# Optimization experiments

Measured on AMD Instinct MI355X. Metric: run time of the kernel, lower is better.

The kernel has to match this reference:

```python
import jax, jax.numpy as jnp
import numpy as np

E = 64        # num_local_experts
N = 32768     # total permuted tokens
H = 1024      # hidden_dim
F = 1024      # intermediate_dim
C = N // E    # per-expert capacity (setup uses equal token counts)


def setup_inputs() -> dict:
    key = jax.random.key(0)
    k1, k2, k3, k4 = jax.random.split(key, 4)
    s = 0.02  # init scale
    return {
        "permuted_local_hidden_states": jax.random.normal(k1, (N, H), jnp.float32),
        "tokens_per_expert": jnp.full((E,), C, dtype=jnp.int32),
        "w_gate": jax.random.normal(k2, (E, H, F), jnp.float32) * s,
        "w_up": jax.random.normal(k3, (E, H, F), jnp.float32) * s,
        "w_down": jax.random.normal(k4, (E, F, H), jnp.float32) * s,
    }


def reference(permuted_local_hidden_states, tokens_per_expert, w_gate, w_up, w_down):
    x = permuted_local_hidden_states  # [N, H], sorted by expert
    counts = tokens_per_expert.astype(jnp.int32)  # [E]
    # start offset of each expert's contiguous token range (torch cumsum + cat([0]))
    starts = jnp.concatenate([jnp.zeros((1,), jnp.int32), jnp.cumsum(counts)])[:-1]
    # expert id and within-expert position for every token (jit-friendly dispatch)
    eid = jnp.repeat(jnp.arange(E, dtype=jnp.int32), counts, total_repeat_length=N)
    pos = jnp.arange(N, dtype=jnp.int32) - starts[eid]
    # gather tokens into fixed-capacity per-expert buffer [E, C, H]; unused slots stay 0
    buf = jnp.zeros((E, C, H), x.dtype).at[eid, pos].set(x)
    # grouped LLaMA MLP: down( silu(gate(x)) * up(x) ), one GEMM triple per expert, batched
    gate = jnp.einsum('ech,ehf->ecf', buf, w_gate)
    up = jnp.einsum('ech,ehf->ecf', buf, w_up)
    h = jax.nn.silu(gate) * up                      # [E, C, F]
    out_buf = jnp.einsum('ecf,efh->ech', h, w_down)  # [E, C, H]
    # scatter back to flat token order (output_local[start:end] = output)
    output_local = out_buf[eid, pos]  # [N, H]
    return output_local
```

## Files before the change

### kernel.cpp

```cpp
#include <hip/hip_runtime.h>
#include <stdint.h>


#define NUM_E 64
#define DIM_H 1024
#define DIM_F 1024
#define CAP   512
#define NTOK  32768

typedef short short8 __attribute__((ext_vector_type(8)));
typedef float f32x4 __attribute__((ext_vector_type(4)));

#define VMCNT(n)  asm volatile("s_waitcnt vmcnt(" #n ")" ::: "memory")
#define LGKMCNT0  asm volatile("s_waitcnt lgkmcnt(0)" ::: "memory")
#define SBAR      __builtin_amdgcn_s_barrier()
#define SCHED0    __builtin_amdgcn_sched_barrier(0)

__device__ __forceinline__ uint32_t cvtpk(float lo, float hi) {
  uint32_t r;
  asm("v_cvt_pk_bf16_f32 %0, %1, %2" : "=v"(r) : "v"(lo), "v"(hi));
  return r;
}
__device__ __forceinline__ unsigned short f2bf(float a) {
  uint32_t ua = __builtin_bit_cast(uint32_t, a);
  ua += 0x7FFFu + ((ua >> 16) & 1u);
  return (unsigned short)(ua >> 16);
}
__device__ __forceinline__ void gload_lds16(const void* g, void* l) {
  __builtin_amdgcn_global_load_lds((const __attribute__((address_space(1))) uint32_t*)g,
                                   (__attribute__((address_space(3))) uint32_t*)l, 16, 0, 0);
}

__global__ __launch_bounds__(256) void cvt_kernel(const float* __restrict__ x,
                                                  unsigned short* __restrict__ xbf) {
  size_t i = ((size_t)blockIdx.x * 256 + threadIdx.x) * 8;
  f32x4 a = *reinterpret_cast<const f32x4*>(x + i);
  f32x4 b = *reinterpret_cast<const f32x4*>(x + i + 4);
  int4 o = make_int4((int)cvtpk(a[0], a[1]), (int)cvtpk(a[2], a[3]),
                     (int)cvtpk(b[0], b[1]), (int)cvtpk(b[2], b[3]));
  *reinterpret_cast<int4*>(xbf + i) = o;
}

__global__ __launch_bounds__(512, 2) void gateup_kernel_v3(
    const unsigned short* __restrict__ xbf, const float* __restrict__ wg,
    const float* __restrict__ wu, unsigned short* __restrict__ hout)
{
  __shared__ unsigned char smem[131072];
  const int t = threadIdx.x;
  int bid = blockIdx.x;
  bid = (bid & 7) * 128 + (bid >> 3);
  const int e = bid >> 4, rr = bid & 15, mb = rr >> 3, nb = rr & 7;
  const int row0 = e * CAP + mb * 256;
  const int col0 = nb * 128;
  const unsigned short* Ag = xbf + (size_t)row0 * DIM_H;
  const float* Bgg = wg + (size_t)e * (DIM_H * DIM_F) + col0;
  const float* Bug = wu + (size_t)e * (DIM_H * DIM_F) + col0;

  const int lane = t & 63, wid = t >> 6;
  const int wm = wid >> 1, wn = wid & 1;

  f32x4 accg[4][4], accu[4][4];
  #pragma unroll
  for (int i = 0; i < 4; i++)
    #pragma unroll
    for (int j = 0; j < 4; j++) {
      accg[i][j] = f32x4{0.f, 0.f, 0.f, 0.f};
      accu[i][j] = f32x4{0.f, 0.f, 0.f, 0.f};
    }

  const int bn = t & 127, bkb = (t >> 7) * 16;
  float bg[16], bu[16];

  auto loadB = [&](int k0) {
    #pragma unroll
    for (int i = 0; i < 16; i++) {
      bg[i] = Bgg[(size_t)(k0 + bkb + i) * DIM_F + bn];
      bu[i] = Bug[(size_t)(k0 + bkb + i) * DIM_F + bn];
    }
  };
  auto writeB = [&](int b) {
    const int Bb = 65536 + b * 32768;
    #pragma unroll
    for (int j = 0; j < 4; j++) {
      int off = Bb + bn * 128 + (((bkb + j * 4) * 2) ^ ((bn & 7) << 4));
      *reinterpret_cast<uint2*>(&smem[off]) =
          make_uint2(cvtpk(bg[j*4+0], bg[j*4+1]), cvtpk(bg[j*4+2], bg[j*4+3]));
      *reinterpret_cast<uint2*>(&smem[off + 16384]) =
          make_uint2(cvtpk(bu[j*4+0], bu[j*4+1]), cvtpk(bu[j*4+2], bu[j*4+3]));
    }
  };
  auto loadA = [&](int k0, int buf) {
    #pragma unroll
    for (int j = 0; j < 4; j++) {
      int lin = (j * 512 + t) * 16;
      int r = lin >> 7;
      int q = (lin >> 4) & 7;
      const void* src = (const unsigned char*)Ag + (size_t)r * 2048 + k0 * 2 + ((q ^ (r & 7)) * 16);
      gload_lds16(src, &smem[buf * 32768 + lin]);
    }
  };
  auto compute = [&](int kt) {
    const int Ab = (kt & 1) * 32768;
    const int Bb = 65536 + (kt & 1) * 32768;
    __builtin_amdgcn_s_setprio(1);
    #pragma unroll
    for (int kk = 0; kk < 2; kk++) {
      short8 a[4], bgf[4], buf_[4];
      #pragma unroll
      for (int mi = 0; mi < 4; mi++) {
        int r = wm * 64 + mi * 16 + (lane & 15);
        a[mi] = *reinterpret_cast<const short8*>(
            &smem[Ab + r * 128 + ((kk * 64 + (lane >> 4) * 16) ^ ((r & 7) << 4))]);
      }
      #pragma unroll
      for (int ni = 0; ni < 4; ni++) {
        int n = wn * 64 + ni * 16 + (lane & 15);
        int off = Bb + n * 128 + ((kk * 64 + (lane >> 4) * 16) ^ ((n & 7) << 4));
        bgf[ni]  = *reinterpret_cast<const short8*>(&smem[off]);
        buf_[ni] = *reinterpret_cast<const short8*>(&smem[off + 16384]);
      }
      #pragma unroll
      for (int mi = 0; mi < 4; mi++)
        #pragma unroll
        for (int ni = 0; ni < 4; ni++) {
          accg[mi][ni] = __builtin_amdgcn_mfma_f32_16x16x32_bf16(a[mi], bgf[ni],  accg[mi][ni], 0, 0, 0);
          accu[mi][ni] = __builtin_amdgcn_mfma_f32_16x16x32_bf16(a[mi], buf_[ni], accu[mi][ni], 0, 0, 0);
        }
    }
    __builtin_amdgcn_s_setprio(0);
  };

  const int NT = DIM_H / 64;
  loadB(0);
  loadA(0, 0);
  VMCNT(4); SCHED0;
  writeB(0);
  LGKMCNT0; VMCNT(0); SCHED0;
  SBAR;
  for (int kt = 0; kt < NT; kt++) {
    if (kt + 1 < NT) {
      loadB((kt + 1) * 64);
      loadA((kt + 1) * 64, (kt + 1) & 1);
      SCHED0;
    }
    compute(kt);
    if (kt + 1 < NT) {
      VMCNT(4); SCHED0;
      writeB((kt + 1) & 1);
      LGKMCNT0; VMCNT(0); SCHED0;
      SBAR;
    }
  }

  #pragma unroll
  for (int mi = 0; mi < 4; mi++)
    #pragma unroll
    for (int ni = 0; ni < 4; ni++) {
      int col = col0 + wn * 64 + ni * 16 + (lane & 15);
      int rbase = row0 + wm * 64 + mi * 16 + (lane >> 4) * 4;
      #pragma unroll
      for (int j = 0; j < 4; j++) {
        float g = accg[mi][ni][j], u = accu[mi][ni][j];
        float hv = (g / (1.f + __expf(-g))) * u;
        hout[(size_t)(rbase + j) * DIM_F + col] = f2bf(hv);
      }
    }
}

__global__ __launch_bounds__(512, 2) void down_kernel_v3(
    const unsigned short* __restrict__ hin, const float* __restrict__ wd,
    float* __restrict__ out)
{
  __shared__ unsigned char smem[98304];
  const int t = threadIdx.x;
  int bid = blockIdx.x;
  bid = (bid & 7) * 128 + (bid >> 3);
  const int e = bid >> 4, rr = bid & 15, mb = rr >> 3, nb = rr & 7;
  const int row0 = e * CAP + mb * 256;
  const int col0 = nb * 128;
  const unsigned short* Ag = hin + (size_t)row0 * DIM_F;
  const float* Bdg = wd + (size_t)e * (DIM_F * DIM_H) + col0;

  const int lane = t & 63, wid = t >> 6;
  const int wm = wid >> 1, wn = wid & 1;

  f32x4 acc[4][4];
  #pragma unroll
  for (int i = 0; i < 4; i++)
    #pragma unroll
    for (int j = 0; j < 4; j++) acc[i][j] = f32x4{0.f, 0.f, 0.f, 0.f};

  const int bn = t & 127, bkb = (t >> 7) * 16;
  float bs[16];

  auto loadB = [&](int k0) {
    #pragma unroll
    for (int i = 0; i < 16; i++)
      bs[i] = Bdg[(size_t)(k0 + bkb + i) * DIM_H + bn];
  };
  auto writeB = [&](int b) {
    const int Bb = 65536 + b * 16384;
    #pragma unroll
    for (int j = 0; j < 4; j++) {
      int off = Bb + bn * 128 + (((bkb + j * 4) * 2) ^ ((bn & 7) << 4));
      *reinterpret_cast<uint2*>(&smem[off]) =
          make_uint2(cvtpk(bs[j*4+0], bs[j*4+1]), cvtpk(bs[j*4+2], bs[j*4+3]));
    }
  };
  auto loadA = [&](int k0, int buf) {
    #pragma unroll
    for (int j = 0; j < 4; j++) {
      int lin = (j * 512 + t) * 16;
      int r = lin >> 7;
      int q = (lin >> 4) & 7;
      const void* src = (const unsigned char*)Ag + (size_t)r * 2048 + k0 * 2 + ((q ^ (r & 7)) * 16);
      gload_lds16(src, &smem[buf * 32768 + lin]);
    }
  };
  auto compute = [&](int kt) {
    const int Ab = (kt & 1) * 32768;
    const int Bb = 65536 + (kt & 1) * 16384;
    __builtin_amdgcn_s_setprio(1);
    #pragma unroll
    for (int kk = 0; kk < 2; kk++) {
      short8 a[4], b[4];
      #pragma unroll
      for (int mi = 0; mi < 4; mi++) {
        int r = wm * 64 + mi * 16 + (lane & 15);
        a[mi] = *reinterpret_cast<const short8*>(
            &smem[Ab + r * 128 + ((kk * 64 + (lane >> 4) * 16) ^ ((r & 7) << 4))]);
      }
      #pragma unroll
      for (int ni = 0; ni < 4; ni++) {
        int n = wn * 64 + ni * 16 + (lane & 15);
        b[ni] = *reinterpret_cast<const short8*>(
            &smem[Bb + n * 128 + ((kk * 64 + (lane >> 4) * 16) ^ ((n & 7) << 4))]);
      }
      #pragma unroll
      for (int mi = 0; mi < 4; mi++)
        #pragma unroll
        for (int ni = 0; ni < 4; ni++)
          acc[mi][ni] = __builtin_amdgcn_mfma_f32_16x16x32_bf16(a[mi], b[ni], acc[mi][ni], 0, 0, 0);
    }
    __builtin_amdgcn_s_setprio(0);
  };

  const int NT = DIM_F / 64;
  loadB(0);
  loadA(0, 0);
  VMCNT(4); SCHED0;
  writeB(0);
  LGKMCNT0; VMCNT(0); SCHED0;
  SBAR;
  for (int kt = 0; kt < NT; kt++) {
    if (kt + 1 < NT) {
      loadB((kt + 1) * 64);
      loadA((kt + 1) * 64, (kt + 1) & 1);
      SCHED0;
    }
    compute(kt);
    if (kt + 1 < NT) {
      VMCNT(4); SCHED0;
      writeB((kt + 1) & 1);
      LGKMCNT0; VMCNT(0); SCHED0;
      SBAR;
    }
  }

  #pragma unroll
  for (int mi = 0; mi < 4; mi++)
    #pragma unroll
    for (int ni = 0; ni < 4; ni++) {
      int col = col0 + wn * 64 + ni * 16 + (lane & 15);
      int rbase = row0 + wm * 64 + mi * 16 + (lane >> 4) * 4;
      #pragma unroll
      for (int j = 0; j < 4; j++)
        out[(size_t)(rbase + j) * DIM_H + col] = acc[mi][ni][j];
    }
}

extern "C" void kernel_launch(void* const* d_in, const int* in_sizes, int n_in,
                              void* d_out, int out_size, void* d_ws, size_t ws_size,
                              hipStream_t stream) {
  (void)in_sizes; (void)n_in; (void)out_size; (void)ws_size;
  const float* x  = (const float*)d_in[0];
  const float* wg = (const float*)d_in[2];
  const float* wu = (const float*)d_in[3];
  const float* wd = (const float*)d_in[4];
  unsigned short* h   = (unsigned short*)d_ws;
  unsigned short* xbf = (unsigned short*)((char*)d_ws + (size_t)NTOK * DIM_F * 2);
  float* out = (float*)d_out;

  cvt_kernel<<<dim3((NTOK * DIM_H) / (256 * 8)), dim3(256), 0, stream>>>(x, xbf);
  gateup_kernel_v3<<<dim3(1024), dim3(512), 0, stream>>>(xbf, wg, wu, h);
  down_kernel_v3<<<dim3(1024), dim3(512), 0, stream>>>(h, wd, out);
}
```

Measured before the change: 365.2 us.

## Switch GEMMs to 32x32x16 MFMA and vectorize fp32 weight loads

Both GEMM kernels replace the 16x16x32 bf16 MFMA tiles with 32x32x16 tiles. Each wave now holds 2x2 accumulators of 16 floats, which cuts the number of LDS fragment reads per MFMA FLOP and raises MFMA efficiency. The fp32 weight loads change from scalar per-column loads to float4 vector loads over a 4x4 k-by-n patch, with a transposed write into LDS. The epilogue row and column mapping is rewritten to match the 32x32 output layout, so any mapping mistake would make the output wrong.

New measurement: 405.9 us. 1.11x slower.

```diff
diff --git a/kernel.cpp b/kernel.cpp
--- a/kernel.cpp
+++ b/kernel.cpp
@@ -10,6 +10,7 @@
 
 typedef short short8 __attribute__((ext_vector_type(8)));
 typedef float f32x4 __attribute__((ext_vector_type(4)));
+typedef float f32x16 __attribute__((ext_vector_type(16)));
 
 #define VMCNT(n)  asm volatile("s_waitcnt vmcnt(" #n ")" ::: "memory")
 #define LGKMCNT0  asm volatile("s_waitcnt lgkmcnt(0)" ::: "memory")
@@ -41,7 +42,7 @@
   *reinterpret_cast<int4*>(xbf + i) = o;
 }
 
-__global__ __launch_bounds__(512, 2) void gateup_kernel_v3(
+__global__ __launch_bounds__(512, 2) void gateup_kernel_v4(
     const unsigned short* __restrict__ xbf, const float* __restrict__ wg,
     const float* __restrict__ wu, unsigned short* __restrict__ hout)
 {
@@ -59,34 +60,36 @@
   const int lane = t & 63, wid = t >> 6;
   const int wm = wid >> 1, wn = wid & 1;
 
-  f32x4 accg[4][4], accu[4][4];
+  f32x16 accg[2][2], accu[2][2];
   #pragma unroll
-  for (int i = 0; i < 4; i++)
-    #pragma unroll
-    for (int j = 0; j < 4; j++) {
-      accg[i][j] = f32x4{0.f, 0.f, 0.f, 0.f};
-      accu[i][j] = f32x4{0.f, 0.f, 0.f, 0.f};
-    }
-
-  const int bn = t & 127, bkb = (t >> 7) * 16;
-  float bg[16], bu[16];
+  for (int i = 0; i < 2; i++)
+    #pragma unroll
+    for (int j = 0; j < 2; j++) {
+      accg[i][j] = (f32x16)(0.f);
+      accu[i][j] = (f32x16)(0.f);
+    }
+
+  const int kg = t & 15, ng = t >> 4;
+  f32x4 vg[4], vu[4];
 
   auto loadB = [&](int k0) {
     #pragma unroll
-    for (int i = 0; i < 16; i++) {
-      bg[i] = Bgg[(size_t)(k0 + bkb + i) * DIM_F + bn];
-      bu[i] = Bug[(size_t)(k0 + bkb + i) * DIM_F + bn];
+    for (int i = 0; i < 4; i++) {
+      size_t off = (size_t)(k0 + kg * 4 + i) * DIM_F + ng * 4;
+      vg[i] = *reinterpret_cast<const f32x4*>(Bgg + off);
+      vu[i] = *reinterpret_cast<const f32x4*>(Bug + off);
     }
   };
   auto writeB = [&](int b) {
     const int Bb = 65536 + b * 32768;
     #pragma unroll
     for (int j = 0; j < 4; j++) {
-      int off = Bb + bn * 128 + (((bkb + j * 4) * 2) ^ ((bn & 7) << 4));
+      int n = ng * 4 + j;
+      int off = Bb + n * 128 + ((kg * 8) ^ ((n & 7) << 4));
       *reinterpret_cast<uint2*>(&smem[off]) =
-          make_uint2(cvtpk(bg[j*4+0], bg[j*4+1]), cvtpk(bg[j*4+2], bg[j*4+3]));
+          make_uint2(cvtpk(vg[0][j], vg[1][j]), cvtpk(vg[2][j], vg[3][j]));
       *reinterpret_cast<uint2*>(&smem[off + 16384]) =
-          make_uint2(cvtpk(bu[j*4+0], bu[j*4+1]), cvtpk(bu[j*4+2], bu[j*4+3]));
+          make_uint2(cvtpk(vu[0][j], vu[1][j]), cvtpk(vu[2][j], vu[3][j]));
     }
   };
   auto loadA = [&](int k0, int buf) {
@@ -104,27 +107,28 @@
     const int Bb = 65536 + (kt & 1) * 32768;
     __builtin_amdgcn_s_setprio(1);
     #pragma unroll
-    for (int kk = 0; kk < 2; kk++) {
-      short8 a[4], bgf[4], buf_[4];
-      #pragma unroll
-      for (int mi = 0; mi < 4; mi++) {
-        int r = wm * 64 + mi * 16 + (lane & 15);
+    for (int kk = 0; kk < 4; kk++) {
+      const int kbyte = kk * 32 + (lane >> 5) * 16;
+      short8 a[2], bgf[2], buf_[2];
+      #pragma unroll
+      for (int mi = 0; mi < 2; mi++) {
+        int r = wm * 64 + mi * 32 + (lane & 31);
         a[mi] = *reinterpret_cast<const short8*>(
-            &smem[Ab + r * 128 + ((kk * 64 + (lane >> 4) * 16) ^ ((r & 7) << 4))]);
-      }
-      #pragma unroll
-      for (int ni = 0; ni < 4; ni++) {
-        int n = wn * 64 + ni * 16 + (lane & 15);
-        int off = Bb + n * 128 + ((kk * 64 + (lane >> 4) * 16) ^ ((n & 7) << 4));
-        bgf[ni]  = *reinterpret_cast<const short8*>(&smem[off]);
-        buf_[ni] = *reinterpret_cast<const short8*>(&smem[off + 16384]);
-      }
-      #pragma unroll
-      for (int mi = 0; mi < 4; mi++)
+            &smem[Ab + r * 128 + (kbyte ^ ((r & 7) << 4))]);
+      }
+      #pragma unroll
+      for (int nj = 0; nj < 2; nj++) {
+        int n = wn * 64 + nj * 32 + (lane & 31);
+        int off = Bb + n * 128 + (kbyte ^ ((n & 7) << 4));
+        bgf[nj]  = *reinterpret_cast<const short8*>(&smem[off]);
+        buf_[nj] = *reinterpret_cast<const short8*>(&smem[off + 16384]);
+      }
+      #pragma unroll
+      for (int mi = 0; mi < 2; mi++)
         #pragma unroll
-        for (int ni = 0; ni < 4; ni++) {
-          accg[mi][ni] = __builtin_amdgcn_mfma_f32_16x16x32_bf16(a[mi], bgf[ni],  accg[mi][ni], 0, 0, 0);
-          accu[mi][ni] = __builtin_amdgcn_mfma_f32_16x16x32_bf16(a[mi], buf_[ni], accu[mi][ni], 0, 0, 0);
+        for (int nj = 0; nj < 2; nj++) {
+          accg[mi][nj] = __builtin_amdgcn_mfma_f32_32x32x16_bf16(a[mi], bgf[nj],  accg[mi][nj], 0, 0, 0);
+          accu[mi][nj] = __builtin_amdgcn_mfma_f32_32x32x16_bf16(a[mi], buf_[nj], accu[mi][nj], 0, 0, 0);
         }
     }
     __builtin_amdgcn_s_setprio(0);
@@ -153,21 +157,22 @@
   }
 
   #pragma unroll
-  for (int mi = 0; mi < 4; mi++)
-    #pragma unroll
-    for (int ni = 0; ni < 4; ni++) {
-      int col = col0 + wn * 64 + ni * 16 + (lane & 15);
-      int rbase = row0 + wm * 64 + mi * 16 + (lane >> 4) * 4;
-      #pragma unroll
-      for (int j = 0; j < 4; j++) {
-        float g = accg[mi][ni][j], u = accu[mi][ni][j];
+  for (int mi = 0; mi < 2; mi++)
+    #pragma unroll
+    for (int nj = 0; nj < 2; nj++) {
+      int col = col0 + wn * 64 + nj * 32 + (lane & 31);
+      int rbase = row0 + wm * 64 + mi * 32 + 4 * (lane >> 5);
+      #pragma unroll
+      for (int reg = 0; reg < 16; reg++) {
+        int row = rbase + (reg & 3) + 8 * (reg >> 2);
+        float g = accg[mi][nj][reg], u = accu[mi][nj][reg];
         float hv = (g / (1.f + __expf(-g))) * u;
-        hout[(size_t)(rbase + j) * DIM_F + col] = f2bf(hv);
-      }
-    }
-}
-
-__global__ __launch_bounds__(512, 2) void down_kernel_v3(
+        hout[(size_t)row * DIM_F + col] = f2bf(hv);
+      }
+    }
+}
+
+__global__ __launch_bounds__(512, 2) void down_kernel_v4(
     const unsigned short* __restrict__ hin, const float* __restrict__ wd,
     float* __restrict__ out)
 {
@@ -184,27 +189,28 @@
   const int lane = t & 63, wid = t >> 6;
   const int wm = wid >> 1, wn = wid & 1;
 
-  f32x4 acc[4][4];
+  f32x16 acc[2][2];
   #pragma unroll
-  for (int i = 0; i < 4; i++)
-    #pragma unroll
-    for (int j = 0; j < 4; j++) acc[i][j] = f32x4{0.f, 0.f, 0.f, 0.f};
-
-  const int bn = t & 127, bkb = (t >> 7) * 16;
-  float bs[16];
+  for (int i = 0; i < 2; i++)
+    #pragma unroll
+    for (int j = 0; j < 2; j++) acc[i][j] = (f32x16)(0.f);
+
+  const int kg = t & 15, ng = t >> 4;
+  f32x4 vb[4];
 
   auto loadB = [&](int k0) {
     #pragma unroll
-    for (int i = 0; i < 16; i++)
-      bs[i] = Bdg[(size_t)(k0 + bkb + i) * DIM_H + bn];
+    for (int i = 0; i < 4; i++)
+      vb[i] = *reinterpret_cast<const f32x4*>(Bdg + (size_t)(k0 + kg * 4 + i) * DIM_H + ng * 4);
   };
   auto writeB = [&](int b) {
     const int Bb = 65536 + b * 16384;
     #pragma unroll
     for (int j = 0; j < 4; j++) {
-      int off = Bb + bn * 128 + (((bkb + j * 4) * 2) ^ ((bn & 7) << 4));
+      int n = ng * 4 + j;
+      int off = Bb + n * 128 + ((kg * 8) ^ ((n & 7) << 4));
       *reinterpret_cast<uint2*>(&smem[off]) =
-          make_uint2(cvtpk(bs[j*4+0], bs[j*4+1]), cvtpk(bs[j*4+2], bs[j*4+3]));
+          make_uint2(cvtpk(vb[0][j], vb[1][j]), cvtpk(vb[2][j], vb[3][j]));
     }
   };
   auto loadA = [&](int k0, int buf) {
@@ -222,25 +228,26 @@
     const int Bb = 65536 + (kt & 1) * 16384;
     __builtin_amdgcn_s_setprio(1);
     #pragma unroll
-    for (int kk = 0; kk < 2; kk++) {
-      short8 a[4], b[4];
-      #pragma unroll
-      for (int mi = 0; mi < 4; mi++) {
-        int r = wm * 64 + mi * 16 + (lane & 15);
+    for (int kk = 0; kk < 4; kk++) {
+      const int kbyte = kk * 32 + (lane >> 5) * 16;
+      short8 a[2], b[2];
+      #pragma unroll
+      for (int mi = 0; mi < 2; mi++) {
+        int r = wm * 64 + mi * 32 + (lane & 31);
         a[mi] = *reinterpret_cast<const short8*>(
-            &smem[Ab + r * 128 + ((kk * 64 + (lane >> 4) * 16) ^ ((r & 7) << 4))]);
-      }
-      #pragma unroll
-      for (int ni = 0; ni < 4; ni++) {
-        int n = wn * 64 + ni * 16 + (lane & 15);
-        b[ni] = *reinterpret_cast<const short8*>(
-            &smem[Bb + n * 128 + ((kk * 64 + (lane >> 4) * 16) ^ ((n & 7) << 4))]);
-      }
-      #pragma unroll
-      for (int mi = 0; mi < 4; mi++)
+            &smem[Ab + r * 128 + (kbyte ^ ((r & 7) << 4))]);
+      }
+      #pragma unroll
+      for (int nj = 0; nj < 2; nj++) {
+        int n = wn * 64 + nj * 32 + (lane & 31);
+        b[nj] = *reinterpret_cast<const short8*>(
+            &smem[Bb + n * 128 + (kbyte ^ ((n & 7) << 4))]);
+      }
+      #pragma unroll
+      for (int mi = 0; mi < 2; mi++)
         #pragma unroll
-        for (int ni = 0; ni < 4; ni++)
-          acc[mi][ni] = __builtin_amdgcn_mfma_f32_16x16x32_bf16(a[mi], b[ni], acc[mi][ni], 0, 0, 0);
+        for (int nj = 0; nj < 2; nj++)
+          acc[mi][nj] = __builtin_amdgcn_mfma_f32_32x32x16_bf16(a[mi], b[nj], acc[mi][nj], 0, 0, 0);
     }
     __builtin_amdgcn_s_setprio(0);
   };
@@ -268,14 +275,16 @@
   }
 
   #pragma unroll
-  for (int mi = 0; mi < 4; mi++)
-    #pragma unroll
-    for (int ni = 0; ni < 4; ni++) {
-      int col = col0 + wn * 64 + ni * 16 + (lane & 15);
-      int rbase = row0 + wm * 64 + mi * 16 + (lane >> 4) * 4;
-      #pragma unroll
-      for (int j = 0; j < 4; j++)
-        out[(size_t)(rbase + j) * DIM_H + col] = acc[mi][ni][j];
+  for (int mi = 0; mi < 2; mi++)
+    #pragma unroll
+    for (int nj = 0; nj < 2; nj++) {
+      int col = col0 + wn * 64 + nj * 32 + (lane & 31);
+      int rbase = row0 + wm * 64 + mi * 32 + 4 * (lane >> 5);
+      #pragma unroll
+      for (int reg = 0; reg < 16; reg++) {
+        int row = rbase + (reg & 3) + 8 * (reg >> 2);
+        out[(size_t)row * DIM_H + col] = acc[mi][nj][reg];
+      }
     }
 }
 
@@ -292,6 +301,6 @@
   float* out = (float*)d_out;
 
   cvt_kernel<<<dim3((NTOK * DIM_H) / (256 * 8)), dim3(256), 0, stream>>>(x, xbf);
-  gateup_kernel_v3<<<dim3(1024), dim3(512), 0, stream>>>(xbf, wg, wu, h);
-  down_kernel_v3<<<dim3(1024), dim3(512), 0, stream>>>(h, wd, out);
-}
+  gateup_kernel_v4<<<dim3(1024), dim3(512), 0, stream>>>(xbf, wg, wu, h);
+  down_kernel_v4<<<dim3(1024), dim3(512), 0, stream>>>(h, wd, out);
+}
```

## Load A fragments directly to registers and vectorize fp32 weight loads

Applied to the files above, without the earlier changes.

Both GEMM kernels stop staging the activation tile in LDS via global_load_lds and instead load A fragments straight from global memory into registers, double-buffered across two k-steps. The weight loads switch from scalar per-column loads to float4 loads along N, with a k-group by n-group thread mapping and a matching swizzled LDS write. This cuts the LDS footprint and LDS traffic and should make weight fetches more coalesced. In exchange it drops the explicit vmcnt/sched_barrier pipelining in favor of compiler scheduling and __syncthreads, raises register pressure, and A reads are no longer shared between warps in LDS, so the duplicated A traffic goes through the caches.

After: 1.251 ms. +242.5%, slower.

```diff
diff --git a/kernel.cpp b/kernel.cpp
--- a/kernel.cpp
+++ b/kernel.cpp
@@ -11,11 +11,6 @@
 typedef short short8 __attribute__((ext_vector_type(8)));
 typedef float f32x4 __attribute__((ext_vector_type(4)));
 
-#define VMCNT(n)  asm volatile("s_waitcnt vmcnt(" #n ")" ::: "memory")
-#define LGKMCNT0  asm volatile("s_waitcnt lgkmcnt(0)" ::: "memory")
-#define SBAR      __builtin_amdgcn_s_barrier()
-#define SCHED0    __builtin_amdgcn_sched_barrier(0)
-
 __device__ __forceinline__ uint32_t cvtpk(float lo, float hi) {
   uint32_t r;
   asm("v_cvt_pk_bf16_f32 %0, %1, %2" : "=v"(r) : "v"(lo), "v"(hi));
@@ -25,10 +20,6 @@
   uint32_t ua = __builtin_bit_cast(uint32_t, a);
   ua += 0x7FFFu + ((ua >> 16) & 1u);
   return (unsigned short)(ua >> 16);
-}
-__device__ __forceinline__ void gload_lds16(const void* g, void* l) {
-  __builtin_amdgcn_global_load_lds((const __attribute__((address_space(1))) uint32_t*)g,
-                                   (__attribute__((address_space(3))) uint32_t*)l, 16, 0, 0);
 }
 
 __global__ __launch_bounds__(256) void cvt_kernel(const float* __restrict__ x,
@@ -41,11 +32,11 @@
   *reinterpret_cast<int4*>(xbf + i) = o;
 }
 
-__global__ __launch_bounds__(512, 2) void gateup_kernel_v3(
+__global__ __launch_bounds__(512, 2) void gateup_kernel_v5(
     const unsigned short* __restrict__ xbf, const float* __restrict__ wg,
     const float* __restrict__ wu, unsigned short* __restrict__ hout)
 {
-  __shared__ unsigned char smem[131072];
+  __shared__ unsigned char smem[65536];
   const int t = threadIdx.x;
   int bid = blockIdx.x;
   bid = (bid & 7) * 128 + (bid >> 3);
@@ -68,50 +59,45 @@
       accu[i][j] = f32x4{0.f, 0.f, 0.f, 0.f};
     }
 
-  const int bn = t & 127, bkb = (t >> 7) * 16;
-  float bg[16], bu[16];
+  const int kg = t & 15, ng = t >> 4;
+  f32x4 vg[4], vu[4];
 
   auto loadB = [&](int k0) {
     #pragma unroll
-    for (int i = 0; i < 16; i++) {
-      bg[i] = Bgg[(size_t)(k0 + bkb + i) * DIM_F + bn];
-      bu[i] = Bug[(size_t)(k0 + bkb + i) * DIM_F + bn];
+    for (int i = 0; i < 4; i++) {
+      size_t off = (size_t)(k0 + kg * 4 + i) * DIM_F + ng * 4;
+      vg[i] = *reinterpret_cast<const f32x4*>(Bgg + off);
+      vu[i] = *reinterpret_cast<const f32x4*>(Bug + off);
     }
   };
   auto writeB = [&](int b) {
-    const int Bb = 65536 + b * 32768;
+    const int Bb = b * 32768;
     #pragma unroll
     for (int j = 0; j < 4; j++) {
-      int off = Bb + bn * 128 + (((bkb + j * 4) * 2) ^ ((bn & 7) << 4));
+      int n = ng * 4 + j;
+      int off = Bb + n * 128 + ((kg * 8) ^ ((n & 7) << 4));
       *reinterpret_cast<uint2*>(&smem[off]) =
-          make_uint2(cvtpk(bg[j*4+0], bg[j*4+1]), cvtpk(bg[j*4+2], bg[j*4+3]));
+          make_uint2(cvtpk(vg[0][j], vg[1][j]), cvtpk(vg[2][j], vg[3][j]));
       *reinterpret_cast<uint2*>(&smem[off + 16384]) =
-          make_uint2(cvtpk(bu[j*4+0], bu[j*4+1]), cvtpk(bu[j*4+2], bu[j*4+3]));
-    }
-  };
-  auto loadA = [&](int k0, int buf) {
-    #pragma unroll
-    for (int j = 0; j < 4; j++) {
-      int lin = (j * 512 + t) * 16;
-      int r = lin >> 7;
-      int q = (lin >> 4) & 7;
-      const void* src = (const unsigned char*)Ag + (size_t)r * 2048 + k0 * 2 + ((q ^ (r & 7)) * 16);
-      gload_lds16(src, &smem[buf * 32768 + lin]);
-    }
-  };
-  auto compute = [&](int kt) {
-    const int Ab = (kt & 1) * 32768;
-    const int Bb = 65536 + (kt & 1) * 32768;
+          make_uint2(cvtpk(vu[0][j], vu[1][j]), cvtpk(vu[2][j], vu[3][j]));
+    }
+  };
+  auto ldA = [&](int k0, short8 (&dst)[8]) {
+    #pragma unroll
+    for (int mi = 0; mi < 4; mi++) {
+      int row = wm * 64 + mi * 16 + (lane & 15);
+      const unsigned short* base = Ag + (size_t)row * DIM_H + k0 + ((lane >> 4) & 3) * 8;
+      #pragma unroll
+      for (int kk = 0; kk < 2; kk++)
+        dst[mi * 2 + kk] = *reinterpret_cast<const short8*>(base + kk * 32);
+    }
+  };
+  auto compute = [&](int b, const short8 (&a)[8]) {
+    const int Bb = b * 32768;
     __builtin_amdgcn_s_setprio(1);
     #pragma unroll
     for (int kk = 0; kk < 2; kk++) {
-      short8 a[4], bgf[4], buf_[4];
-      #pragma unroll
-      for (int mi = 0; mi < 4; mi++) {
-        int r = wm * 64 + mi * 16 + (lane & 15);
-        a[mi] = *reinterpret_cast<const short8*>(
-            &smem[Ab + r * 128 + ((kk * 64 + (lane >> 4) * 16) ^ ((r & 7) << 4))]);
-      }
+      short8 bgf[4], buf_[4];
       #pragma unroll
       for (int ni = 0; ni < 4; ni++) {
         int n = wn * 64 + ni * 16 + (lane & 15);
@@ -123,33 +109,34 @@
       for (int mi = 0; mi < 4; mi++)
         #pragma unroll
         for (int ni = 0; ni < 4; ni++) {
-          accg[mi][ni] = __builtin_amdgcn_mfma_f32_16x16x32_bf16(a[mi], bgf[ni],  accg[mi][ni], 0, 0, 0);
-          accu[mi][ni] = __builtin_amdgcn_mfma_f32_16x16x32_bf16(a[mi], buf_[ni], accu[mi][ni], 0, 0, 0);
+          accg[mi][ni] = __builtin_amdgcn_mfma_f32_16x16x32_bf16(a[mi*2+kk], bgf[ni],  accg[mi][ni], 0, 0, 0);
+          accu[mi][ni] = __builtin_amdgcn_mfma_f32_16x16x32_bf16(a[mi*2+kk], buf_[ni], accu[mi][ni], 0, 0, 0);
         }
     }
     __builtin_amdgcn_s_setprio(0);
   };
 
+  short8 a0[8], a1[8];
   const int NT = DIM_H / 64;
   loadB(0);
-  loadA(0, 0);
-  VMCNT(4); SCHED0;
+  ldA(0, a0);
   writeB(0);
-  LGKMCNT0; VMCNT(0); SCHED0;
-  SBAR;
-  for (int kt = 0; kt < NT; kt++) {
-    if (kt + 1 < NT) {
-      loadB((kt + 1) * 64);
-      loadA((kt + 1) * 64, (kt + 1) & 1);
-      SCHED0;
-    }
-    compute(kt);
-    if (kt + 1 < NT) {
-      VMCNT(4); SCHED0;
-      writeB((kt + 1) & 1);
-      LGKMCNT0; VMCNT(0); SCHED0;
-      SBAR;
-    }
+  __syncthreads();
+  #pragma unroll 1
+  for (int it = 0; it < NT / 2; it++) {
+    const int kt1 = it * 2 + 1;
+    loadB(kt1 * 64);
+    ldA(kt1 * 64, a1);
+    compute(0, a0);
+    writeB(1);
+    __syncthreads();
+    if (kt1 + 1 < NT) {
+      loadB((kt1 + 1) * 64);
+      ldA((kt1 + 1) * 64, a0);
+    }
+    compute(1, a1);
+    if (kt1 + 1 < NT) writeB(0);
+    __syncthreads();
   }
 
   #pragma unroll
@@ -167,11 +154,11 @@
     }
 }
 
-__global__ __launch_bounds__(512, 2) void down_kernel_v3(
+__global__ __launch_bounds__(512, 2) void down_kernel_v5(
     const unsigned short* __restrict__ hin, const float* __restrict__ wd,
     float* __restrict__ out)
 {
-  __shared__ unsigned char smem[98304];
+  __shared__ unsigned char smem[32768];
   const int t = threadIdx.x;
   int bid = blockIdx.x;
   bid = (bid & 7) * 128 + (bid >> 3);
@@ -190,81 +177,76 @@
     #pragma unroll
     for (int j = 0; j < 4; j++) acc[i][j] = f32x4{0.f, 0.f, 0.f, 0.f};
 
-  const int bn = t & 127, bkb = (t >> 7) * 16;
-  float bs[16];
+  const int kg = t & 15, ng = t >> 4;
+  f32x4 vb[4];
 
   auto loadB = [&](int k0) {
     #pragma unroll
-    for (int i = 0; i < 16; i++)
-      bs[i] = Bdg[(size_t)(k0 + bkb + i) * DIM_H + bn];
+    for (int i = 0; i < 4; i++)
+      vb[i] = *reinterpret_cast<const f32x4*>(Bdg + (size_t)(k0 + kg * 4 + i) * DIM_H + ng * 4);
   };
   auto writeB = [&](int b) {
-    const int Bb = 65536 + b * 16384;
+    const int Bb = b * 16384;
     #pragma unroll
     for (int j = 0; j < 4; j++) {
-      int off = Bb + bn * 128 + (((bkb + j * 4) * 2) ^ ((bn & 7) << 4));
+      int n = ng * 4 + j;
+      int off = Bb + n * 128 + ((kg * 8) ^ ((n & 7) << 4));
       *reinterpret_cast<uint2*>(&smem[off]) =
-          make_uint2(cvtpk(bs[j*4+0], bs[j*4+1]), cvtpk(bs[j*4+2], bs[j*4+3]));
-    }
-  };
-  auto loadA = [&](int k0, int buf) {
-    #pragma unroll
-    for (int j = 0; j < 4; j++) {
-      int lin = (j * 512 + t) * 16;
-      int r = lin >> 7;
-      int q = (lin >> 4) & 7;
-      const void* src = (const unsigned char*)Ag + (size_t)r * 2048 + k0 * 2 + ((q ^ (r & 7)) * 16);
-      gload_lds16(src, &smem[buf * 32768 + lin]);
-    }
-  };
-  auto compute = [&](int kt) {
-    const int Ab = (kt & 1) * 32768;
-    const int Bb = 65536 + (kt & 1) * 16384;
+          make_uint2(cvtpk(vb[0][j], vb[1][j]), cvtpk(vb[2][j], vb[3][j]));
+    }
+  };
+  auto ldA = [&](int k0, short8 (&dst)[8]) {
+    #pragma unroll
+    for (int mi = 0; mi < 4; mi++) {
+      int row = wm * 64 + mi * 16 + (lane & 15);
+      const unsigned short* base = Ag + (size_t)row * DIM_F + k0 + ((lane >> 4) & 3) * 8;
+      #pragma unroll
+      for (int kk = 0; kk < 2; kk++)
+        dst[mi * 2 + kk] = *reinterpret_cast<const short8*>(base + kk * 32);
+    }
+  };
+  auto compute = [&](int b, const short8 (&a)[8]) {
+    const int Bb = b * 16384;
     __builtin_amdgcn_s_setprio(1);
     #pragma unroll
     for (int kk = 0; kk < 2; kk++) {
-      short8 a[4], b[4];
-      #pragma unroll
-      for (int mi = 0; mi < 4; mi++) {
-        int r = wm * 64 + mi * 16 + (lane & 15);
-        a[mi] = *reinterpret_cast<const short8*>(
-            &smem[Ab + r * 128 + ((kk * 64 + (lane >> 4) * 16) ^ ((r & 7) << 4))]);
-      }
+      short8 bf[4];
       #pragma unroll
       for (int ni = 0; ni < 4; ni++) {
         int n = wn * 64 + ni * 16 + (lane & 15);
-        b[ni] = *reinterpret_cast<const short8*>(
+        bf[ni] = *reinterpret_cast<const short8*>(
             &smem[Bb + n * 128 + ((kk * 64 + (lane >> 4) * 16) ^ ((n & 7) << 4))]);
       }
       #pragma unroll
       for (int mi = 0; mi < 4; mi++)
         #pragma unroll
         for (int ni = 0; ni < 4; ni++)
-          acc[mi][ni] = __builtin_amdgcn_mfma_f32_16x16x32_bf16(a[mi], b[ni], acc[mi][ni], 0, 0, 0);
+          acc[mi][ni] = __builtin_amdgcn_mfma_f32_16x16x32_bf16(a[mi*2+kk], bf[ni], acc[mi][ni], 0, 0, 0);
     }
     __builtin_amdgcn_s_setprio(0);
   };
 
+  short8 a0[8], a1[8];
   const int NT = DIM_F / 64;
   loadB(0);
-  loadA(0, 0);
-  VMCNT(4); SCHED0;
+  ldA(0, a0);
   writeB(0);
-  LGKMCNT0; VMCNT(0); SCHED0;
-  SBAR;
-  for (int kt = 0; kt < NT; kt++) {
-    if (kt + 1 < NT) {
-      loadB((kt + 1) * 64);
-      loadA((kt + 1) * 64, (kt + 1) & 1);
-      SCHED0;
-    }
-    compute(kt);
-    if (kt + 1 < NT) {
-      VMCNT(4); SCHED0;
-      writeB((kt + 1) & 1);
-      LGKMCNT0; VMCNT(0); SCHED0;
-      SBAR;
-    }
+  __syncthreads();
+  #pragma unroll 1
+  for (int it = 0; it < NT / 2; it++) {
+    const int kt1 = it * 2 + 1;
+    loadB(kt1 * 64);
+    ldA(kt1 * 64, a1);
+    compute(0, a0);
+    writeB(1);
+    __syncthreads();
+    if (kt1 + 1 < NT) {
+      loadB((kt1 + 1) * 64);
+      ldA((kt1 + 1) * 64, a0);
+    }
+    compute(1, a1);
+    if (kt1 + 1 < NT) writeB(0);
+    __syncthreads();
   }
 
   #pragma unroll
@@ -292,6 +274,6 @@
   float* out = (float*)d_out;
 
   cvt_kernel<<<dim3((NTOK * DIM_H) / (256 * 8)), dim3(256), 0, stream>>>(x, xbf);
-  gateup_kernel_v3<<<dim3(1024), dim3(512), 0, stream>>>(xbf, wg, wu, h);
-  down_kernel_v3<<<dim3(1024), dim3(512), 0, stream>>>(h, wd, out);
-}
+  gateup_kernel_v5<<<dim3(1024), dim3(512), 0, stream>>>(xbf, wg, wu, h);
+  down_kernel_v5<<<dim3(1024), dim3(512), 0, stream>>>(h, wd, out);
+}
```

## Deepen B prefetch to two stages and interleave MFMA with loads

Applied to the files above, without the earlier changes.

Both GEMM kernels now keep two register sets of fp32 weight tiles, so the global B load for tile k+2 is issued while tile k is computed. B is now read as float2 vectors per thread along n with 8 k-rows, and written to LDS as 16-byte stores instead of 8-byte ones. The main loop is unrolled by two and split into finer MFMA phases, with A LDS-DMA loads and B writes placed between them, to hide global latency behind matrix work. In exchange, register pressure rises with the extra prefetch buffers, and the vmcnt bookkeeping becomes more fragile.

Result: slower. 1.321 ms (+261.6%).

```diff
diff --git a/kernel.cpp b/kernel.cpp
--- a/kernel.cpp
+++ b/kernel.cpp
@@ -9,12 +9,15 @@
 #define NTOK  32768
 
 typedef short short8 __attribute__((ext_vector_type(8)));
+typedef float f32x2 __attribute__((ext_vector_type(2)));
 typedef float f32x4 __attribute__((ext_vector_type(4)));
 
 #define VMCNT(n)  asm volatile("s_waitcnt vmcnt(" #n ")" ::: "memory")
 #define LGKMCNT0  asm volatile("s_waitcnt lgkmcnt(0)" ::: "memory")
 #define SBAR      __builtin_amdgcn_s_barrier()
 #define SCHED0    __builtin_amdgcn_sched_barrier(0)
+#define SP1       __builtin_amdgcn_s_setprio(1)
+#define SP0       __builtin_amdgcn_s_setprio(0)
 
 __device__ __forceinline__ uint32_t cvtpk(float lo, float hi) {
   uint32_t r;
@@ -41,7 +44,7 @@
   *reinterpret_cast<int4*>(xbf + i) = o;
 }
 
-__global__ __launch_bounds__(512, 2) void gateup_kernel_v3(
+__global__ __launch_bounds__(512, 2) void gateup_kernel_v7(
     const unsigned short* __restrict__ xbf, const float* __restrict__ wg,
     const float* __restrict__ wu, unsigned short* __restrict__ hout)
 {
@@ -68,25 +71,30 @@
       accu[i][j] = f32x4{0.f, 0.f, 0.f, 0.f};
     }
 
-  const int bn = t & 127, bkb = (t >> 7) * 16;
-  float bg[16], bu[16];
-
-  auto loadB = [&](int k0) {
-    #pragma unroll
-    for (int i = 0; i < 16; i++) {
-      bg[i] = Bgg[(size_t)(k0 + bkb + i) * DIM_F + bn];
-      bu[i] = Bug[(size_t)(k0 + bkb + i) * DIM_F + bn];
-    }
-  };
-  auto writeB = [&](int b) {
+  const int kb = (t & 7) * 8;
+  const int n2 = (t >> 3) * 2;
+  f32x2 g0[8], u0[8], g1[8], u1[8];
+
+  auto loadB = [&](int k0, f32x2 (&g)[8], f32x2 (&u)[8]) {
+    #pragma unroll
+    for (int i = 0; i < 8; i++) {
+      size_t off = (size_t)(k0 + kb + i) * DIM_F + n2;
+      g[i] = *reinterpret_cast<const f32x2*>(Bgg + off);
+      u[i] = *reinterpret_cast<const f32x2*>(Bug + off);
+    }
+  };
+  auto writeB = [&](int b, const f32x2 (&g)[8], const f32x2 (&u)[8]) {
     const int Bb = 65536 + b * 32768;
     #pragma unroll
-    for (int j = 0; j < 4; j++) {
-      int off = Bb + bn * 128 + (((bkb + j * 4) * 2) ^ ((bn & 7) << 4));
-      *reinterpret_cast<uint2*>(&smem[off]) =
-          make_uint2(cvtpk(bg[j*4+0], bg[j*4+1]), cvtpk(bg[j*4+2], bg[j*4+3]));
-      *reinterpret_cast<uint2*>(&smem[off + 16384]) =
-          make_uint2(cvtpk(bu[j*4+0], bu[j*4+1]), cvtpk(bu[j*4+2], bu[j*4+3]));
+    for (int j = 0; j < 2; j++) {
+      int n = n2 + j;
+      int off = Bb + n * 128 + ((kb * 2) ^ ((n & 7) << 4));
+      *reinterpret_cast<int4*>(&smem[off]) =
+          make_int4((int)cvtpk(g[0][j], g[1][j]), (int)cvtpk(g[2][j], g[3][j]),
+                    (int)cvtpk(g[4][j], g[5][j]), (int)cvtpk(g[6][j], g[7][j]));
+      *reinterpret_cast<int4*>(&smem[off + 16384]) =
+          make_int4((int)cvtpk(u[0][j], u[1][j]), (int)cvtpk(u[2][j], u[3][j]),
+                    (int)cvtpk(u[4][j], u[5][j]), (int)cvtpk(u[6][j], u[7][j]));
     }
   };
   auto loadA = [&](int k0, int buf) {
@@ -99,55 +107,83 @@
       gload_lds16(src, &smem[buf * 32768 + lin]);
     }
   };
-  auto compute = [&](int kt) {
-    const int Ab = (kt & 1) * 32768;
-    const int Bb = 65536 + (kt & 1) * 32768;
-    __builtin_amdgcn_s_setprio(1);
-    #pragma unroll
-    for (int kk = 0; kk < 2; kk++) {
-      short8 a[4], bgf[4], buf_[4];
+  auto ldsA = [&](short8 (&a)[4], int Ab, int kk) {
+    #pragma unroll
+    for (int mi = 0; mi < 4; mi++) {
+      int r = wm * 64 + mi * 16 + (lane & 15);
+      a[mi] = *reinterpret_cast<const short8*>(
+          &smem[Ab + r * 128 + ((kk * 64 + (lane >> 4) * 16) ^ ((r & 7) << 4))]);
+    }
+  };
+  auto ldsB = [&](short8 (&bb)[4], int Bb, int kk, int uoff) {
+    #pragma unroll
+    for (int ni = 0; ni < 4; ni++) {
+      int n = wn * 64 + ni * 16 + (lane & 15);
+      bb[ni] = *reinterpret_cast<const short8*>(
+          &smem[Bb + uoff + n * 128 + ((kk * 64 + (lane >> 4) * 16) ^ ((n & 7) << 4))]);
+    }
+  };
+  auto mf16 = [&](f32x4 (&acc)[4][4], const short8 (&a)[4], const short8 (&bb)[4]) {
+    SP1;
+    #pragma unroll
+    for (int mi = 0; mi < 4; mi++)
       #pragma unroll
-      for (int mi = 0; mi < 4; mi++) {
-        int r = wm * 64 + mi * 16 + (lane & 15);
-        a[mi] = *reinterpret_cast<const short8*>(
-            &smem[Ab + r * 128 + ((kk * 64 + (lane >> 4) * 16) ^ ((r & 7) << 4))]);
-      }
-      #pragma unroll
-      for (int ni = 0; ni < 4; ni++) {
-        int n = wn * 64 + ni * 16 + (lane & 15);
-        int off = Bb + n * 128 + ((kk * 64 + (lane >> 4) * 16) ^ ((n & 7) << 4));
-        bgf[ni]  = *reinterpret_cast<const short8*>(&smem[off]);
-        buf_[ni] = *reinterpret_cast<const short8*>(&smem[off + 16384]);
-      }
-      #pragma unroll
-      for (int mi = 0; mi < 4; mi++)
-        #pragma unroll
-        for (int ni = 0; ni < 4; ni++) {
-          accg[mi][ni] = __builtin_amdgcn_mfma_f32_16x16x32_bf16(a[mi], bgf[ni],  accg[mi][ni], 0, 0, 0);
-          accu[mi][ni] = __builtin_amdgcn_mfma_f32_16x16x32_bf16(a[mi], buf_[ni], accu[mi][ni], 0, 0, 0);
-        }
-    }
-    __builtin_amdgcn_s_setprio(0);
+      for (int ni = 0; ni < 4; ni++)
+        acc[mi][ni] = __builtin_amdgcn_mfma_f32_16x16x32_bf16(a[mi], bb[ni], acc[mi][ni], 0, 0, 0);
+    SP0;
   };
 
   const int NT = DIM_H / 64;
-  loadB(0);
+  loadB(0, g0, u0);
   loadA(0, 0);
+  SCHED0;
   VMCNT(4); SCHED0;
-  writeB(0);
-  LGKMCNT0; VMCNT(0); SCHED0;
+  writeB(0, g0, u0);
+  loadB(64, g1, u1);
+  SCHED0;
+  VMCNT(16); LGKMCNT0; SCHED0;
   SBAR;
-  for (int kt = 0; kt < NT; kt++) {
-    if (kt + 1 < NT) {
-      loadB((kt + 1) * 64);
-      loadA((kt + 1) * 64, (kt + 1) & 1);
+
+  #pragma unroll 1
+  for (int it = 0; it < 8; it++) {
+    const int kt0 = it * 2, kt1 = kt0 + 1;
+    const bool more = (it < 7);
+    short8 a[4], bb[4];
+    ldsA(a, 0, 0); ldsB(bb, 65536, 0, 0);
+    mf16(accg, a, bb);
+    loadA(kt0 * 64 + 64, 1);
+    SCHED0;
+    ldsB(bb, 65536, 0, 16384);
+    mf16(accu, a, bb);
+    VMCNT(4); SCHED0;
+    writeB(1, g1, u1);
+    if (more) loadB(kt0 * 64 + 128, g0, u0);
+    SCHED0;
+    ldsA(a, 0, 1); ldsB(bb, 65536, 1, 0);
+    mf16(accg, a, bb);
+    ldsB(bb, 65536, 1, 16384);
+    mf16(accu, a, bb);
+    if (more) { VMCNT(16); } else { VMCNT(0); }
+    LGKMCNT0; SCHED0;
+    SBAR;
+    ldsA(a, 32768, 0); ldsB(bb, 98304, 0, 0);
+    mf16(accg, a, bb);
+    if (more) loadA(kt1 * 64 + 64, 0);
+    SCHED0;
+    ldsB(bb, 98304, 0, 16384);
+    mf16(accu, a, bb);
+    if (more) {
+      VMCNT(4); SCHED0;
+      writeB(0, g0, u0);
+      loadB(kt1 * 64 + 128, g1, u1);
       SCHED0;
     }
-    compute(kt);
-    if (kt + 1 < NT) {
-      VMCNT(4); SCHED0;
-      writeB((kt + 1) & 1);
-      LGKMCNT0; VMCNT(0); SCHED0;
+    ldsA(a, 32768, 1); ldsB(bb, 98304, 1, 0);
+    mf16(accg, a, bb);
+    ldsB(bb, 98304, 1, 16384);
+    mf16(accu, a, bb);
+    if (more) {
+      VMCNT(16); LGKMCNT0; SCHED0;
       SBAR;
     }
   }
@@ -160,14 +196,14 @@
       int rbase = row0 + wm * 64 + mi * 16 + (lane >> 4) * 4;
       #pragma unroll
       for (int j = 0; j < 4; j++) {
-        float g = accg[mi][ni][j], u = accu[mi][ni][j];
-        float hv = (g / (1.f + __expf(-g))) * u;
+        float gv = accg[mi][ni][j], uv = accu[mi][ni][j];
+        float hv = (gv / (1.f + __expf(-gv))) * uv;
         hout[(size_t)(rbase + j) * DIM_F + col] = f2bf(hv);
       }
     }
 }
 
-__global__ __launch_bounds__(512, 2) void down_kernel_v3(
+__global__ __launch_bounds__(512, 2) void down_kernel_v7(
     const unsigned short* __restrict__ hin, const float* __restrict__ wd,
     float* __restrict__ out)
 {
@@ -190,21 +226,24 @@
     #pragma unroll
     for (int j = 0; j < 4; j++) acc[i][j] = f32x4{0.f, 0.f, 0.f, 0.f};
 
-  const int bn = t & 127, bkb = (t >> 7) * 16;
-  float bs[16];
-
-  auto loadB = [&](int k0) {
-    #pragma unroll
-    for (int i = 0; i < 16; i++)
-      bs[i] = Bdg[(size_t)(k0 + bkb + i) * DIM_H + bn];
-  };
-  auto writeB = [&](int b) {
+  const int kb = (t & 7) * 8;
+  const int n2 = (t >> 3) * 2;
+  f32x2 b0[8], b1[8];
+
+  auto loadB = [&](int k0, f32x2 (&bv)[8]) {
+    #pragma unroll
+    for (int i = 0; i < 8; i++)
+      bv[i] = *reinterpret_cast<const f32x2*>(Bdg + (size_t)(k0 + kb + i) * DIM_H + n2);
+  };
+  auto writeB = [&](int b, const f32x2 (&bv)[8]) {
     const int Bb = 65536 + b * 16384;
     #pragma unroll
-    for (int j = 0; j < 4; j++) {
-      int off = Bb + bn * 128 + (((bkb + j * 4) * 2) ^ ((bn & 7) << 4));
-      *reinterpret_cast<uint2*>(&smem[off]) =
-          make_uint2(cvtpk(bs[j*4+0], bs[j*4+1]), cvtpk(bs[j*4+2], bs[j*4+3]));
+    for (int j = 0; j < 2; j++) {
+      int n = n2 + j;
+      int off = Bb + n * 128 + ((kb * 2) ^ ((n & 7) << 4));
+      *reinterpret_cast<int4*>(&smem[off]) =
+          make_int4((int)cvtpk(bv[0][j], bv[1][j]), (int)cvtpk(bv[2][j], bv[3][j]),
+                    (int)cvtpk(bv[4][j], bv[5][j]), (int)cvtpk(bv[6][j], bv[7][j]));
     }
   };
   auto loadA = [&](int k0, int buf) {
@@ -217,52 +256,84 @@
       gload_lds16(src, &smem[buf * 32768 + lin]);
     }
   };
-  auto compute = [&](int kt) {
-    const int Ab = (kt & 1) * 32768;
-    const int Bb = 65536 + (kt & 1) * 16384;
-    __builtin_amdgcn_s_setprio(1);
-    #pragma unroll
-    for (int kk = 0; kk < 2; kk++) {
-      short8 a[4], b[4];
+  auto ldsA = [&](short8 (&a)[4], int Ab, int kk) {
+    #pragma unroll
+    for (int mi = 0; mi < 4; mi++) {
+      int r = wm * 64 + mi * 16 + (lane & 15);
+      a[mi] = *reinterpret_cast<const short8*>(
+          &smem[Ab + r * 128 + ((kk * 64 + (lane >> 4) * 16) ^ ((r & 7) << 4))]);
+    }
+  };
+  auto ldsBh = [&](short8 (&bb)[2], int Bb, int kk, int half) {
+    #pragma unroll
+    for (int i = 0; i < 2; i++) {
+      int n = wn * 64 + (half * 2 + i) * 16 + (lane & 15);
+      bb[i] = *reinterpret_cast<const short8*>(
+          &smem[Bb + n * 128 + ((kk * 64 + (lane >> 4) * 16) ^ ((n & 7) << 4))]);
+    }
+  };
+  auto mf8 = [&](const short8 (&a)[4], const short8 (&bb)[2], int half) {
+    SP1;
+    #pragma unroll
+    for (int mi = 0; mi < 4; mi++)
       #pragma unroll
-      for (int mi = 0; mi < 4; mi++) {
-        int r = wm * 64 + mi * 16 + (lane & 15);
-        a[mi] = *reinterpret_cast<const short8*>(
-            &smem[Ab + r * 128 + ((kk * 64 + (lane >> 4) * 16) ^ ((r & 7) << 4))]);
-      }
-      #pragma unroll
-      for (int ni = 0; ni < 4; ni++) {
-        int n = wn * 64 + ni * 16 + (lane & 15);
-        b[ni] = *reinterpret_cast<const short8*>(
-            &smem[Bb + n * 128 + ((kk * 64 + (lane >> 4) * 16) ^ ((n & 7) << 4))]);
-      }
-      #pragma unroll
-      for (int mi = 0; mi < 4; mi++)
-        #pragma unroll
-        for (int ni = 0; ni < 4; ni++)
-          acc[mi][ni] = __builtin_amdgcn_mfma_f32_16x16x32_bf16(a[mi], b[ni], acc[mi][ni], 0, 0, 0);
-    }
-    __builtin_amdgcn_s_setprio(0);
+      for (int i = 0; i < 2; i++)
+        acc[mi][half * 2 + i] =
+            __builtin_amdgcn_mfma_f32_16x16x32_bf16(a[mi], bb[i], acc[mi][half * 2 + i], 0, 0, 0);
+    SP0;
   };
 
   const int NT = DIM_F / 64;
-  loadB(0);
+  loadB(0, b0);
   loadA(0, 0);
+  SCHED0;
   VMCNT(4); SCHED0;
-  writeB(0);
-  LGKMCNT0; VMCNT(0); SCHED0;
+  writeB(0, b0);
+  loadB(64, b1);
+  SCHED0;
+  VMCNT(8); LGKMCNT0; SCHED0;
   SBAR;
-  for (int kt = 0; kt < NT; kt++) {
-    if (kt + 1 < NT) {
-      loadB((kt + 1) * 64);
-      loadA((kt + 1) * 64, (kt + 1) & 1);
+
+  #pragma unroll 1
+  for (int it = 0; it < 8; it++) {
+    const int kt0 = it * 2, kt1 = kt0 + 1;
+    const bool more = (it < 7);
+    short8 a[4], bb[2];
+    ldsA(a, 0, 0); ldsBh(bb, 65536, 0, 0);
+    mf8(a, bb, 0);
+    loadA(kt0 * 64 + 64, 1);
+    SCHED0;
+    ldsBh(bb, 65536, 0, 1);
+    mf8(a, bb, 1);
+    VMCNT(4); SCHED0;
+    writeB(1, b1);
+    if (more) loadB(kt0 * 64 + 128, b0);
+    SCHED0;
+    ldsA(a, 0, 1); ldsBh(bb, 65536, 1, 0);
+    mf8(a, bb, 0);
+    ldsBh(bb, 65536, 1, 1);
+    mf8(a, bb, 1);
+    if (more) { VMCNT(8); } else { VMCNT(0); }
+    LGKMCNT0; SCHED0;
+    SBAR;
+    ldsA(a, 32768, 0); ldsBh(bb, 81920, 0, 0);
+    mf8(a, bb, 0);
+    if (more) loadA(kt1 * 64 + 64, 0);
+    SCHED0;
+    ldsBh(bb, 81920, 0, 1);
+    mf8(a, bb, 1);
+    if (more) {
+      VMCNT(4); SCHED0;
+      writeB(0, b0);
+      loadB(kt1 * 64 + 128, b1);
       SCHED0;
     }
-    compute(kt);
-    if (kt + 1 < NT) {
-      VMCNT(4); SCHED0;
-      writeB((kt + 1) & 1);
-      LGKMCNT0; VMCNT(0); SCHED0;
+    ldsA(a, 32768, 1); ldsBh(bb, 81920, 1, 0);
+    mf8(a, bb, 0);
+    ldsBh(bb, 81920, 1, 1);
+    mf8(a, bb, 1);
+    if (more) {
+      VMCNT(8); LGKMCNT0; SCHED0;
       SBAR;
     }
   }
@@ -292,6 +363,6 @@
   float* out = (float*)d_out;
 
   cvt_kernel<<<dim3((NTOK * DIM_H) / (256 * 8)), dim3(256), 0, stream>>>(x, xbf);
-  gateup_kernel_v3<<<dim3(1024), dim3(512), 0, stream>>>(xbf, wg, wu, h);
-  down_kernel_v3<<<dim3(1024), dim3(512), 0, stream>>>(h, wd, out);
-}
+  gateup_kernel_v7<<<dim3(1024), dim3(512), 0, stream>>>(xbf, wg, wu, h);
+  down_kernel_v7<<<dim3(1024), dim3(512), 0, stream>>>(h, wd, out);
+}
```
